# Kernel optimization log

Measured on AMD Instinct MI355X. Metric: run time of the kernel, lower is better.

The kernel has to match this reference:

```python
import jax, jax.numpy as jnp
import numpy as np

N, D, H, O, E, K = 131072, 512, 512, 512, 8, 2
LN_EPS = 1e-5


def setup_inputs() -> dict:
    key = jax.random.key(0)
    k0, k1, k2, k3 = jax.random.split(key, 4)
    x = jax.random.normal(k0, (N, D), jnp.float32)
    # gate: nn.init.normal_(weight, 0, 0.1); stored as [D, E] (transposed torch layout)
    Wg = jax.random.normal(k1, (D, E), jnp.float32) * 0.1
    # experts: xavier_uniform for fc1/fc2, LayerNorm gamma=1, beta=0
    b1 = float(np.sqrt(6.0 / (D + H)))
    b2 = float(np.sqrt(6.0 / (H + O)))
    W1 = jax.random.uniform(k2, (E, D, H), jnp.float32, -b1, b1)
    W2 = jax.random.uniform(k3, (E, H, O), jnp.float32, -b2, b2)
    gamma = jnp.ones((E, H), jnp.float32)
    beta = jnp.zeros((E, H), jnp.float32)
    return {"x": x, "Wg": Wg, "W1": W1, "gamma": gamma, "beta": beta, "W2": W2}


def _layer_norm(h, g, b):
    mu = jnp.mean(h, axis=-1, keepdims=True)
    var = jnp.mean(jnp.square(h - mu), axis=-1, keepdims=True)  # biased, as torch LayerNorm
    return (h - mu) * jax.lax.rsqrt(var + LN_EPS) * g + b


def reference(x, Wg, W1, gamma, beta, W2):
    n = x.shape[0]
    # gating: softmax over experts (eval mode: no noise, no dropout)
    gating = jax.nn.softmax(x @ Wg, axis=-1)            # [N, E]
    vals, idx = jax.lax.top_k(gating, K)                # [N, K]
    # F.normalize(p=1): values are positive softmax probs -> divide by L1 sum
    vals = vals / jnp.maximum(jnp.sum(vals, axis=-1, keepdims=True), 1e-12)
    # scatter top-k weights into dense per-expert combine weights [N, E]
    cw = jnp.zeros((n, E), x.dtype).at[jnp.arange(n)[:, None], idx].add(vals)
    out = jnp.zeros((n, W2.shape[-1]), x.dtype)
    for e in range(E):  # small fixed loop over experts
        h = jax.nn.gelu(_layer_norm(x @ W1[e], gamma[e], beta[e]), approximate=False)
        out = out + cw[:, e:e + 1] * (h @ W2[e])
    return out
```

## Files before the change

### kernel.cpp

```cpp
#include <hip/hip_runtime.h>
#include <hip/hip_bf16.h>
#include <stdint.h>

#define NTOK 131072
#define NEXP 8

typedef unsigned short ushortT;
typedef __attribute__((ext_vector_type(4))) float f32x4;
typedef __attribute__((ext_vector_type(8))) short s16x8;
typedef __attribute__((ext_vector_type(8))) __bf16 bf16x8;

__device__ __forceinline__ float bfu2f(unsigned short u){
  union { float f; uint32_t i; } c; c.i = ((uint32_t)u) << 16; return c.f;
}
__device__ __forceinline__ unsigned short f2bfu(float f){
  union { float f; uint32_t i; } c; c.f = f;
  uint32_t x = c.i;
  uint32_t r = (x + 0x7fffu + ((x >> 16) & 1u)) >> 16;
  return (unsigned short)r;
}
__device__ __forceinline__ float gelu_f(float x){
  float u = 0.7978845608028654f * (x + 0.044715f * x * x * x);
  float e = __expf(2.0f * u);
  float t = 1.0f - 2.0f / (e + 1.0f);
  return 0.5f * x * (1.0f + t);
}
__device__ __forceinline__ bf16x8 ldfrag(const void* p){
  s16x8 v = *(const s16x8*)p;
  return __builtin_bit_cast(bf16x8, v);
}

__global__ __launch_bounds__(64) void zero_cursors_kernel(int* __restrict__ cursors){
  if (threadIdx.x < 16) cursors[threadIdx.x] = 0;
}

__global__ __launch_bounds__(256) void prep_w_kernel(const float* __restrict__ W1,
                                                     const float* __restrict__ W2,
                                                     ushortT* __restrict__ W1f,
                                                     ushortT* __restrict__ W2f){
  int bid = blockIdx.x;
  const float* src; ushortT* dst;
  if (bid < 512){ src = W1; dst = W1f; } else { src = W2; dst = W2f; bid -= 512; }
  int e  = bid >> 6;
  int kt = (bid >> 3) & 7;
  int nt = bid & 7;
  __shared__ ushortT tileT[64][68];
  int t = threadIdx.x;
  #pragma unroll
  for (int i = 0; i < 16; i++){
    int idx = t + i*256;
    int r = idx >> 6, c = idx & 63;
    float v = src[((size_t)(e*512 + kt*64 + r))*512 + nt*64 + c];
    tileT[c][r] = f2bfu(v);
  }
  __syncthreads();
  int sub = t >> 6, l = t & 63;
  #pragma unroll
  for (int fo = 0; fo < 2; fo++){
    int fr  = sub + fo*4;
    int nbl = fr >> 1;
    int ks  = fr & 1;
    int nb  = nt*4 + nbl;
    size_t fi = ((size_t)(e*32 + nb))*16 + kt*2 + ks;
    ushortT tmp[8];
    #pragma unroll
    for (int j = 0; j < 8; j++)
      tmp[j] = tileT[nbl*16 + (l & 15)][ks*32 + (l >> 4)*8 + j];
    *(s16x8*)(dst + fi*512 + l*8) = *(s16x8*)tmp;
  }
}

__global__ __launch_bounds__(256) void gating_kernel(const float* __restrict__ x,
                                                     const float* __restrict__ Wg,
                                                     ushortT* __restrict__ xbf,
                                                     int* __restrict__ epair,
                                                     float* __restrict__ wt){
  int l = threadIdx.x & 63;
  int wv = threadIdx.x >> 6;
  f32x4 wgv[16];
  #pragma unroll
  for (int i = 0; i < 8; i++){
    const f32x4* p = (const f32x4*)(Wg + (size_t)(l*8 + i)*8);
    wgv[2*i] = p[0]; wgv[2*i+1] = p[1];
  }
  int tbase = (blockIdx.x * 4 + wv) * 16;
  for (int tt = 0; tt < 16; tt++){
    int t = tbase + tt;
    const f32x4* xr = (const f32x4*)(x + (size_t)t*512 + l*8);
    f32x4 xa = xr[0], xb = xr[1];
    float acc[8];
    #pragma unroll
    for (int e2 = 0; e2 < 8; e2++) acc[e2] = 0.f;
    #pragma unroll
    for (int i = 0; i < 4; i++){
      float xi = xa[i], xj = xb[i];
      #pragma unroll
      for (int e2 = 0; e2 < 4; e2++){
        acc[e2]   += xi * wgv[2*i][e2];
        acc[4+e2] += xi * wgv[2*i+1][e2];
        acc[e2]   += xj * wgv[2*(i+4)][e2];
        acc[4+e2] += xj * wgv[2*(i+4)+1][e2];
      }
    }
    #pragma unroll
    for (int off = 1; off < 64; off <<= 1){
      #pragma unroll
      for (int e2 = 0; e2 < 8; e2++) acc[e2] += __shfl_xor(acc[e2], off);
    }
    int e0 = 0; float v0 = acc[0];
    #pragma unroll
    for (int e2 = 1; e2 < 8; e2++) if (acc[e2] > v0){ v0 = acc[e2]; e0 = e2; }
    int e1 = -1; float v1 = -3.4e38f;
    #pragma unroll
    for (int e2 = 0; e2 < 8; e2++){ if (e2 != e0 && acc[e2] > v1){ v1 = acc[e2]; e1 = e2; } }
    float w0 = 1.f / (1.f + __expf(v1 - v0));
    if (l == 0){
      epair[t] = e0 | (e1 << 4);
      wt[t] = w0;
      wt[NTOK + t] = 1.f - w0;
    }
    s16x8 o;
    #pragma unroll
    for (int j = 0; j < 4; j++){ o[j] = (short)f2bfu(xa[j]); o[4+j] = (short)f2bfu(xb[j]); }
    *(s16x8*)(xbf + (size_t)t*512 + l*8) = o;
  }
}

__global__ __launch_bounds__(256) void scatter_kernel(const int* __restrict__ epair,
                                                      int* __restrict__ cursors,
                                                      int* __restrict__ lists){
  __shared__ int cntL[16]; __shared__ int baseL[16];
  int tid = threadIdx.x;
  if (tid < 16) cntL[tid] = 0;
  __syncthreads();
  int t = blockIdx.x * 256 + tid;
  int p = epair[t];
  int e0 = p & 15, e1 = (p >> 4) & 15;
  int lp0 = atomicAdd(&cntL[e0], 1);
  int lp1 = atomicAdd(&cntL[8 + e1], 1);
  __syncthreads();
  if (tid < 16) baseL[tid] = atomicAdd(&cursors[tid], cntL[tid]);
  __syncthreads();
  lists[(size_t)e0 * NTOK + baseL[e0] + lp0] = t;
  lists[(size_t)(8 + e1) * NTOK + baseL[8 + e1] + lp1] = t;
}

template<int SLOT>
__global__ __launch_bounds__(512, 4) void expert_kernel(
    const ushortT* __restrict__ xbf, const ushortT* __restrict__ W1bf,
    const ushortT* __restrict__ W2bf, const float* __restrict__ gamma,
    const float* __restrict__ beta, const float* __restrict__ wt,
    const int* __restrict__ cursors, const int* __restrict__ lists,
    float* __restrict__ out)
{
  __shared__ ushortT hX[64 * 512];
  __shared__ int   toksL[64];
  __shared__ float wrowL[64];
  __shared__ float wsumL[8][64];
  __shared__ float wsqL[8][64];
  __shared__ float muL[64];
  __shared__ float rsL[64];

  int tid = threadIdx.x;
  int w = tid >> 6;
  int l = tid & 63;

  int bid = (int)blockIdx.x;
  bid = (bid & 7) * 257 + (bid >> 3);

  int e = -1, tile = 0, bacc = 0, cn = 0;
  #pragma unroll
  for (int i = 0; i < 8; i++){
    int c = cursors[SLOT*8 + i];
    int ntl = (c + 63) >> 6;
    if (e < 0 && bid < bacc + ntl){ e = i; tile = bid - bacc; cn = c; }
    bacc += ntl;
  }
  if (e < 0) return;
  int tb = tile * 64;
  const int* lbase = lists + (size_t)(SLOT*8 + e) * NTOK;

  if (tid < 64){
    int idx = tb + tid;
    int tok = (idx < cn) ? lbase[idx] : -1;
    toksL[tid] = tok;
    wrowL[tid] = (tok >= 0) ? wt[(size_t)SLOT*NTOK + tok] : 0.f;
  }

  {
    int r = tid >> 3, cs = tid & 7;
    int idx = tb + r; if (idx >= cn) idx = tb;
    int tokS = lbase[idx];
    const int4* xrow = (const int4*)(xbf + (size_t)tokS * 512);
    #pragma unroll
    for (int half = 0; half < 2; half++){
      int4 xv[4];
      #pragma unroll
      for (int i = 0; i < 4; i++) xv[i] = xrow[cs + (half*4 + i)*8];
      #pragma unroll
      for (int i = 0; i < 4; i++){
        int slot = cs + (half*4 + i)*8;
        int ss = slot ^ (r & 7);
        *(int4*)((char*)hX + r*1024 + ss*16) = xv[i];
      }
    }
  }
  __syncthreads();

  const int aB0 = (l & 15)*1024 + ((((l >> 4)    ) ^ (l & 7)) << 4);
  const int aB1 = (l & 15)*1024 + (((4 + (l >> 4)) ^ (l & 7)) << 4);
  const char* Xp = (const char*)hX;

  const ushortT* w1f = W1bf + ((size_t)(e*32 + w*4))*16*512;
  const ushortT* w2f = W2bf + ((size_t)(e*32 + w*4))*16*512;

  f32x4 acc[4][4];

#define LOADB(dst, wf, s_) { \
    _Pragma("unroll") \
    for (int nf = 0; nf < 4; nf++) \
      dst[nf] = ldfrag((wf) + ((nf*16 + (s_)) << 9) + (l << 3)); }
#define LOADA(dst, s_) { \
    const int ab_ = ((s_) & 1) ? aB1 : aB0; \
    _Pragma("unroll") \
    for (int m = 0; m < 4; m++) \
      dst[m] = ldfrag(Xp + ab_ + m*16384 + ((s_) >> 1)*128); }
#define MFMAS(Aa, Bb) { \
    _Pragma("unroll") \
    for (int nf = 0; nf < 4; nf++) \
      _Pragma("unroll") \
      for (int m = 0; m < 4; m++) \
        acc[m][nf] = __builtin_amdgcn_mfma_f32_16x16x32_bf16(Aa[m], Bb[nf], acc[m][nf], 0, 0, 0); }

  #pragma unroll
  for (int m = 0; m < 4; m++)
    #pragma unroll
    for (int nf = 0; nf < 4; nf++) acc[m][nf] = (f32x4){0.f,0.f,0.f,0.f};
  {
    bf16x8 Ba[4], Bb[4];
    LOADB(Ba, w1f, 0);
    #pragma unroll
    for (int s = 0; s < 16; s += 2){
      { bf16x8 A[4]; LOADA(A, s);
        LOADB(Bb, w1f, s+1);
        MFMAS(A, Ba); }
      { bf16x8 A[4]; LOADA(A, s+1);
        if (s+2 < 16) LOADB(Ba, w1f, s+2);
        MFMAS(A, Bb); }
    }
  }

  #pragma unroll
  for (int m = 0; m < 4; m++){
    #pragma unroll
    for (int j = 0; j < 4; j++){
      float s = acc[m][0][j] + acc[m][1][j] + acc[m][2][j] + acc[m][3][j];
      float q = acc[m][0][j]*acc[m][0][j] + acc[m][1][j]*acc[m][1][j]
              + acc[m][2][j]*acc[m][2][j] + acc[m][3][j]*acc[m][3][j];
      s += __shfl_xor(s, 1); q += __shfl_xor(q, 1);
      s += __shfl_xor(s, 2); q += __shfl_xor(q, 2);
      s += __shfl_xor(s, 4); q += __shfl_xor(q, 4);
      s += __shfl_xor(s, 8); q += __shfl_xor(q, 8);
      if ((l & 15) == 0){
        int row = m*16 + (l >> 4)*4 + j;
        wsumL[w][row] = s;
        wsqL[w][row]  = q;
      }
    }
  }
  __syncthreads();

  if (tid < 64){
    float s = 0.f, q = 0.f;
    #pragma unroll
    for (int i = 0; i < 8; i++){ s += wsumL[i][tid]; q += wsqL[i][tid]; }
    float mu = s * (1.f/512.f);
    float var = q * (1.f/512.f) - mu*mu;
    muL[tid] = mu;
    rsL[tid] = rsqrtf(var + 1e-5f);
  }
  __syncthreads();

  {
    #pragma unroll
    for (int m = 0; m < 4; m++){
      #pragma unroll
      for (int j = 0; j < 4; j++){
        int row = m*16 + (l >> 4)*4 + j;
        float mu = muL[row], rs = rsL[row];
        #pragma unroll
        for (int nf = 0; nf < 4; nf++){
          int col = w*64 + nf*16 + (l & 15);
          float g = gamma[e*512 + col];
          float b = beta [e*512 + col];
          float v = (acc[m][nf][j] - mu) * rs * g + b;
          v = gelu_f(v);
          int ss = (col >> 3) ^ (row & 7);
          *(ushortT*)((char*)hX + row*1024 + ss*16 + (col & 7)*2) = f2bfu(v);
        }
      }
    }
  }
  __syncthreads();

  #pragma unroll
  for (int m = 0; m < 4; m++)
    #pragma unroll
    for (int nf = 0; nf < 4; nf++) acc[m][nf] = (f32x4){0.f,0.f,0.f,0.f};
  {
    bf16x8 Ba[4], Bb[4];
    LOADB(Ba, w2f, 0);
    #pragma unroll
    for (int s = 0; s < 16; s += 2){
      { bf16x8 A[4]; LOADA(A, s);
        LOADB(Bb, w2f, s+1);
        MFMAS(A, Ba); }
      { bf16x8 A[4]; LOADA(A, s+1);
        if (s+2 < 16) LOADB(Ba, w2f, s+2);
        MFMAS(A, Bb); }
    }
  }

  #pragma unroll
  for (int m = 0; m < 4; m++){
    #pragma unroll
    for (int j = 0; j < 4; j++){
      int row = m*16 + (l >> 4)*4 + j;
      int tok = toksL[row];
      if (tok >= 0){
        float wr = wrowL[row];
        #pragma unroll
        for (int nf = 0; nf < 4; nf++){
          int col = w*64 + nf*16 + (l & 15);
          float val = acc[m][nf][j] * wr;
          float* p = out + (size_t)tok*512 + col;
          if (SLOT == 0) *p = val; else *p += val;
        }
      }
    }
  }
#undef LOADB
#undef LOADA
#undef MFMAS
}

extern "C" void kernel_launch(void* const* d_in, const int* in_sizes, int n_in,
                              void* d_out, int out_size, void* d_ws, size_t ws_size,
                              hipStream_t stream){
  const float* x     = (const float*)d_in[0];
  const float* Wg    = (const float*)d_in[1];
  const float* W1    = (const float*)d_in[2];
  const float* gamma = (const float*)d_in[3];
  const float* beta  = (const float*)d_in[4];
  const float* W2    = (const float*)d_in[5];
  float* out = (float*)d_out;

  char* ws = (char*)d_ws;
  size_t off = 0;
  ushortT* xbf   = (ushortT*)(ws + off); off += (size_t)NTOK*512*2;
  ushortT* W1bf  = (ushortT*)(ws + off); off += (size_t)8*512*512*2;
  ushortT* W2bf  = (ushortT*)(ws + off); off += (size_t)8*512*512*2;
  int*     lists = (int*)(ws + off);     off += (size_t)16*NTOK*4;
  float*   wtp   = (float*)(ws + off);   off += (size_t)2*NTOK*4;
  int*     epair = (int*)(ws + off);     off += (size_t)NTOK*4;
  int*     cursors = (int*)(ws + off);   off += 256;

  zero_cursors_kernel<<<1, 64, 0, stream>>>(cursors);
  prep_w_kernel<<<1024, 256, 0, stream>>>(W1, W2, W1bf, W2bf);
  gating_kernel<<<NTOK/64, 256, 0, stream>>>(x, Wg, xbf, epair, wtp);
  scatter_kernel<<<NTOK/256, 256, 0, stream>>>(epair, cursors, lists);
  expert_kernel<0><<<2056, 512, 0, stream>>>(xbf, W1bf, W2bf, gamma, beta, wtp, cursors, lists, out);
  expert_kernel<1><<<2056, 512, 0, stream>>>(xbf, W1bf, W2bf, gamma, beta, wtp, cursors, lists, out);
}
```

Baseline: 748.4 us.

## Stage expert weight fragments through LDS via async global_load_lds double buffer

Weight B-fragments for both expert GEMMs are no longer loaded from global into registers. They are now staged asynchronously into a double-buffered 64KB LDS region with global_load_lds, prefetching the next k-step while the current one computes. The W2 first stage is also issued during the last W1 step. Launch bounds drop from 4 to 2 blocks per CU to fit the extra LDS, and gamma/beta loads are hoisted out of the inner loop. This adds a block barrier per k-step and lowers occupancy. There is also a possible race, since async LDS writes are not explicitly waited on before the ldfrag reads.

```diff
diff --git a/kernel.cpp b/kernel.cpp
--- a/kernel.cpp
+++ b/kernel.cpp
@@ -29,6 +29,10 @@
   s16x8 v = *(const s16x8*)p;
   return __builtin_bit_cast(bf16x8, v);
 }
+
+#define GLOAD16(g_, l_) \
+  __builtin_amdgcn_global_load_lds((const __attribute__((address_space(1))) uint32_t*)(g_), \
+                                   (__attribute__((address_space(3))) uint32_t*)(l_), 16, 0, 0)
 
 __global__ __launch_bounds__(64) void zero_cursors_kernel(int* __restrict__ cursors){
   if (threadIdx.x < 16) cursors[threadIdx.x] = 0;
@@ -146,7 +150,7 @@
 }
 
 template<int SLOT>
-__global__ __launch_bounds__(512, 4) void expert_kernel(
+__global__ __launch_bounds__(512, 2) void expert_kernel(
     const ushortT* __restrict__ xbf, const ushortT* __restrict__ W1bf,
     const ushortT* __restrict__ W2bf, const float* __restrict__ gamma,
     const float* __restrict__ beta, const float* __restrict__ wt,
@@ -154,6 +158,7 @@
     float* __restrict__ out)
 {
   __shared__ ushortT hX[64 * 512];
+  __shared__ ushortT Wb[2][16384];
   __shared__ int   toksL[64];
   __shared__ float wrowL[64];
   __shared__ float wsumL[8][64];
@@ -180,6 +185,18 @@
   int tb = tile * 64;
   const int* lbase = lists + (size_t)(SLOT*8 + e) * NTOK;
 
+  const ushortT* w1base = W1bf + ((size_t)e*32)*16*512;
+  const ushortT* w2base = W2bf + ((size_t)e*32)*16*512;
+
+#define STAGEW(wfb_, b_, s_) { \
+    _Pragma("unroll") \
+    for (int nf_ = 0; nf_ < 4; nf_++){ \
+      const ushortT* gs_ = (wfb_) + ((size_t)(((w*4 + nf_)*16 + (s_))) << 9) + (l << 3); \
+      GLOAD16(gs_, &Wb[b_][(w*4 + nf_) << 9]); \
+    } }
+
+  STAGEW(w1base, 0, 0);
+
   if (tid < 64){
     int idx = tb + tid;
     int tok = (idx < cn) ? lbase[idx] : -1;
@@ -211,43 +228,36 @@
   const int aB1 = (l & 15)*1024 + (((4 + (l >> 4)) ^ (l & 7)) << 4);
   const char* Xp = (const char*)hX;
 
-  const ushortT* w1f = W1bf + ((size_t)(e*32 + w*4))*16*512;
-  const ushortT* w2f = W2bf + ((size_t)(e*32 + w*4))*16*512;
-
   f32x4 acc[4][4];
 
-#define LOADB(dst, wf, s_) { \
-    _Pragma("unroll") \
-    for (int nf = 0; nf < 4; nf++) \
-      dst[nf] = ldfrag((wf) + ((nf*16 + (s_)) << 9) + (l << 3)); }
-#define LOADA(dst, s_) { \
-    const int ab_ = ((s_) & 1) ? aB1 : aB0; \
-    _Pragma("unroll") \
-    for (int m = 0; m < 4; m++) \
-      dst[m] = ldfrag(Xp + ab_ + m*16384 + ((s_) >> 1)*128); }
-#define MFMAS(Aa, Bb) { \
+#define MFMAS() { \
     _Pragma("unroll") \
     for (int nf = 0; nf < 4; nf++) \
       _Pragma("unroll") \
       for (int m = 0; m < 4; m++) \
-        acc[m][nf] = __builtin_amdgcn_mfma_f32_16x16x32_bf16(Aa[m], Bb[nf], acc[m][nf], 0, 0, 0); }
+        acc[m][nf] = __builtin_amdgcn_mfma_f32_16x16x32_bf16(A[m], B[nf], acc[m][nf], 0, 0, 0); }
 
   #pragma unroll
   for (int m = 0; m < 4; m++)
     #pragma unroll
     for (int nf = 0; nf < 4; nf++) acc[m][nf] = (f32x4){0.f,0.f,0.f,0.f};
-  {
-    bf16x8 Ba[4], Bb[4];
-    LOADB(Ba, w1f, 0);
-    #pragma unroll
-    for (int s = 0; s < 16; s += 2){
-      { bf16x8 A[4]; LOADA(A, s);
-        LOADB(Bb, w1f, s+1);
-        MFMAS(A, Ba); }
-      { bf16x8 A[4]; LOADA(A, s+1);
-        if (s+2 < 16) LOADB(Ba, w1f, s+2);
-        MFMAS(A, Bb); }
-    }
+
+  for (int s = 0; s < 16; s++){
+    int cur = s & 1;
+    if (s < 15) STAGEW(w1base, cur ^ 1, s + 1)
+    else        STAGEW(w2base, 0, 0)
+    bf16x8 B[4], A[4];
+    #pragma unroll
+    for (int nf = 0; nf < 4; nf++)
+      B[nf] = ldfrag(&Wb[cur][((w*4 + nf) << 9) + (l << 3)]);
+    {
+      const int ab = (s & 1) ? aB1 : aB0;
+      #pragma unroll
+      for (int m = 0; m < 4; m++)
+        A[m] = ldfrag(Xp + ab + m*16384 + (s >> 1)*128);
+    }
+    MFMAS();
+    __syncthreads();
   }
 
   #pragma unroll
@@ -282,6 +292,13 @@
   __syncthreads();
 
   {
+    float g[4], b[4];
+    #pragma unroll
+    for (int nf = 0; nf < 4; nf++){
+      int col = w*64 + nf*16 + (l & 15);
+      g[nf] = gamma[e*512 + col];
+      b[nf] = beta [e*512 + col];
+    }
     #pragma unroll
     for (int m = 0; m < 4; m++){
       #pragma unroll
@@ -291,9 +308,7 @@
         #pragma unroll
         for (int nf = 0; nf < 4; nf++){
           int col = w*64 + nf*16 + (l & 15);
-          float g = gamma[e*512 + col];
-          float b = beta [e*512 + col];
-          float v = (acc[m][nf][j] - mu) * rs * g + b;
+          float v = (acc[m][nf][j] - mu) * rs * g[nf] + b[nf];
           v = gelu_f(v);
           int ss = (col >> 3) ^ (row & 7);
           *(ushortT*)((char*)hX + row*1024 + ss*16 + (col & 7)*2) = f2bfu(v);
@@ -307,18 +322,22 @@
   for (int m = 0; m < 4; m++)
     #pragma unroll
     for (int nf = 0; nf < 4; nf++) acc[m][nf] = (f32x4){0.f,0.f,0.f,0.f};
-  {
-    bf16x8 Ba[4], Bb[4];
-    LOADB(Ba, w2f, 0);
-    #pragma unroll
-    for (int s = 0; s < 16; s += 2){
-      { bf16x8 A[4]; LOADA(A, s);
-        LOADB(Bb, w2f, s+1);
-        MFMAS(A, Ba); }
-      { bf16x8 A[4]; LOADA(A, s+1);
-        if (s+2 < 16) LOADB(Ba, w2f, s+2);
-        MFMAS(A, Bb); }
-    }
+
+  for (int s = 0; s < 16; s++){
+    int cur = s & 1;
+    if (s < 15) STAGEW(w2base, cur ^ 1, s + 1)
+    bf16x8 B[4], A[4];
+    #pragma unroll
+    for (int nf = 0; nf < 4; nf++)
+      B[nf] = ldfrag(&Wb[cur][((w*4 + nf) << 9) + (l << 3)]);
+    {
+      const int ab = (s & 1) ? aB1 : aB0;
+      #pragma unroll
+      for (int m = 0; m < 4; m++)
+        A[m] = ldfrag(Xp + ab + m*16384 + (s >> 1)*128);
+    }
+    MFMAS();
+    __syncthreads();
   }
 
   #pragma unroll
@@ -339,8 +358,7 @@
       }
     }
   }
-#undef LOADB
-#undef LOADA
+#undef STAGEW
 #undef MFMAS
 }
 
```

After: 929.4 us. +24.2%, slower.
